# Kernel tuning notes

Measured on AMD Instinct MI355X. Metric: run time of the kernel, lower is better.

## Reference

```python
import jax, jax.numpy as jnp
import numpy as np

S = 160                 # image size (renderer default is 256; reduced for working-set budget)
SIGMA = 1.0             # soft-silhouette sharpness, in pixels
EPS = 1e-8
CHUNK = 512             # faces per rasterization chunk
ANGLE = np.pi / 2.0
VIEW_TAN = float(np.tan(np.radians(30.0)))   # nr.Renderer default viewing_angle=30
CAM_POS = np.array([0.0, 0.0, 2.732], dtype=np.float32)

# constant rotation: Rodrigues formula for axis-angle (pi/2 about y), as in nr.rotation_from_axis
_aa = ANGLE * np.array([0.0, 1.0, 0.0])
_th = np.linalg.norm(_aa)
_k = _aa / _th
_K = np.array([[0, -_k[2], _k[1]], [_k[2], 0, -_k[0]], [-_k[1], _k[0], 0]])
ROT = (np.eye(3) + np.sin(_th) * _K + (1 - np.cos(_th)) * (_K @ _K)).astype(np.float32)


def _make_uv_sphere(stacks=32, slices=64):
    verts = [[0.0, 0.0, 1.0]]
    for i in range(1, stacks):
        phi = np.pi * i / stacks
        for j in range(slices):
            th = 2 * np.pi * j / slices
            verts.append([np.sin(phi) * np.cos(th), np.sin(phi) * np.sin(th), np.cos(phi)])
    verts.append([0.0, 0.0, -1.0])
    V = len(verts)
    faces = []
    for j in range(slices):
        faces.append([0, 1 + j, 1 + (j + 1) % slices])
    for i in range(stacks - 2):
        r0 = 1 + i * slices
        r1 = r0 + slices
        for j in range(slices):
            a, b = r0 + j, r0 + (j + 1) % slices
            c, d = r1 + j, r1 + (j + 1) % slices
            faces.append([a, b, c])
            faces.append([b, d, c])
    r0 = 1 + (stacks - 2) * slices
    for j in range(slices):
        faces.append([V - 1, r0 + (j + 1) % slices, r0 + j])
    return np.asarray(verts, np.float32), np.asarray(faces, np.int32)


def setup_inputs() -> dict:
    key = jax.random.key(0)
    v, f = _make_uv_sphere()                     # V=1986, F=3968
    pad = 4096 - f.shape[0]
    f = np.concatenate([f, np.zeros((pad, 3), np.int32)], axis=0)  # degenerate pad faces
    image_ref = jax.random.uniform(key, (1, S, S), dtype=jnp.float32)
    return {"vertices": jnp.asarray(v)[None], "faces": jnp.asarray(f)[None], "image_ref": image_ref}


def _project(v):
    # world -> camera (rotate, place camera at z=2.732) -> perspective -> pixel coords
    vc = v @ ROT.T + CAM_POS                     # [V,3]
    xy = vc[:, :2] / (vc[:, 2:3] * VIEW_TAN)     # NDC in [-1,1]
    return (xy + 1.0) * (S / 2.0)                # [V,2] pixels


def _soft_coverage(pts, fv):
    # pts [P,2] pixel centers, fv [C,3,2] screen-space triangles -> coverage [P,C]
    a, b, c = fv[:, 0], fv[:, 1], fv[:, 2]

    def edge_dist(p0, p1):
        d = p1 - p0                                              # [C,2]
        cr = d[:, 0] * (pts[:, None, 1] - p0[None, :, 1]) - d[:, 1] * (pts[:, None, 0] - p0[None, :, 0])
        return cr / (jnp.sqrt(jnp.sum(d * d, -1)) + EPS)         # signed pixel distance [P,C]

    area = (b[:, 0] - a[:, 0]) * (c[:, 1] - a[:, 1]) - (b[:, 1] - a[:, 1]) * (c[:, 0] - a[:, 0])
    sg = jnp.where(area >= 0, 1.0, -1.0)[None, :]                # winding correction
    dmin = jnp.minimum(jnp.minimum(edge_dist(a, b) * sg, edge_dist(b, c) * sg), edge_dist(c, a) * sg)
    cov = jax.nn.sigmoid(dmin / SIGMA)
    return cov * (jnp.abs(area) > 1e-6)[None, :]                 # mask degenerate (padded) faces


def reference(vertices, faces, image_ref):
    v2 = _project(vertices[0])                   # [V,2]
    fv = v2[faces[0]]                            # [F,3,2]
    fvc = fv.reshape(-1, CHUNK, 3, 2)            # [F/CHUNK, CHUNK, 3, 2]
    ys, xs = jnp.meshgrid(jnp.arange(S, dtype=jnp.float32) + 0.5,
                          jnp.arange(S, dtype=jnp.float32) + 0.5, indexing="ij")
    pts = jnp.stack([xs.ravel(), ys.ravel()], -1)  # [P,2]

    cov_fn = jax.checkpoint(_soft_coverage)

    def body(not_cov, fvk):
        cov = cov_fn(pts, fvk)                   # [P,CHUNK]
        return not_cov * jnp.prod(1.0 - cov, axis=1), None

    not_cov, _ = jax.lax.scan(body, jnp.ones((S * S,), jnp.float32), fvc)
    images = (1.0 - not_cov).reshape(1, S, S)    # silhouette in [0,1]
    loss = jnp.sum((images - image_ref) ** 2)    # broadcast matches images - image_ref[None] in torch
    return images, loss
```

## Files before the change

kernel.cpp:

```cpp
#include <hip/hip_runtime.h>
#include <math.h>

#define S_IMG 160
#define NPIX (S_IMG * S_IMG)
#define NF 4096
#define NV 1986
#define TS 16
#define NTX 10
#define NTILE 100
#define CAP NF
#define INV_LN2 1.4426950408889634f
#define CULL_THRESH -25.0f

#define ROT_EPS 6.123234e-17f
#define CAM_Z 2.732f
#define VIEW_TAN 0.5773502691896258f

#if __has_builtin(__builtin_amdgcn_exp2f)
#define EXP2F(x) __builtin_amdgcn_exp2f(x)
#else
#define EXP2F(x) exp2f(x)
#endif

__global__ void __launch_bounds__(512) mega(const float* __restrict__ verts,
                                            const int* __restrict__ faces,
                                            float* __restrict__ list,
                                            const float* __restrict__ img_ref,
                                            float* __restrict__ out,
                                            float* __restrict__ bsums) {
    __shared__ float2 sverts[NV];
    __shared__ float4 stage[8][64 * 3];
    __shared__ float pacc[8][256];
    __shared__ float red[8];
    __shared__ int wcnt[8];

    const int t = blockIdx.x;
    const int tid = threadIdx.x;
    const int wid = tid >> 6;
    const int lane = tid & 63;

    for (int i = tid; i < NV; i += 512) {
        float x = verts[3 * i], y = verts[3 * i + 1], z = verts[3 * i + 2];
        float vx = fmaf(ROT_EPS, x, z);
        float vz = fmaf(ROT_EPS, z, -x) + CAM_Z;
        float inv = __builtin_amdgcn_rcpf(vz * VIEW_TAN);
        sverts[i] = make_float2(fmaf(vx * inv, 80.0f, 80.0f),
                                fmaf(y * inv, 80.0f, 80.0f));
    }
    __syncthreads();

    const float cx = (float)((t % NTX) * TS) + 8.0f;
    const float cy = (float)((t / NTX) * TS) + 8.0f;
    float* mylist = list + (size_t)t * CAP * 12;
    int base = 0;

    for (int r = 0; r < NF / 512; ++r) {
        int f = r * 512 + tid;
        int i0 = faces[3 * f], i1 = faces[3 * f + 1], i2 = faces[3 * f + 2];
        float2 a = sverts[i0];
        float2 b = sverts[i1];
        float2 c = sverts[i2];
        float area = (b.x - a.x) * (c.y - a.y) - (b.y - a.y) * (c.x - a.x);
        float sg = (area >= 0.0f) ? INV_LN2 : -INV_LN2;
        bool valid = fabsf(area) > 1e-6f;

        float o[9];
        float umin = 1e30f;
        float2 p0s[3] = {a, b, c};
        float2 p1s[3] = {b, c, a};
#pragma unroll
        for (int e = 0; e < 3; ++e) {
            float dx = p1s[e].x - p0s[e].x;
            float dy = p1s[e].y - p0s[e].y;
            float dd = fmaf(dx, dx, dy * dy);
            float s = sg * __builtin_amdgcn_rsqf(dd);
            float A = valid ? (-dy * s) : 0.0f;
            float B = valid ? (dx * s) : 0.0f;
            float C = valid ? ((dy * p0s[e].x - dx * p0s[e].y) * s) : -1e30f;
            o[3 * e + 0] = A;
            o[3 * e + 1] = B;
            o[3 * e + 2] = C;
            float bound = fmaf(fabsf(A) + fabsf(B), 7.5f, fmaf(A, cx, fmaf(B, cy, C)));
            umin = fminf(umin, valid ? bound : -1e30f);
        }
        bool pred = umin >= CULL_THRESH;
        unsigned long long m = __ballot(pred);
        int wpop = __popcll(m);
        int prefix = __popcll(m & ((1ull << lane) - 1ull));

        __syncthreads();
        if (lane == 0) wcnt[wid] = wpop;
        __syncthreads();
        int off = base;
#pragma unroll
        for (int w = 0; w < 8; ++w) {
            int cw = wcnt[w];
            if (w < wid) off += cw;
            base += cw;
        }
        off += prefix;
        if (pred) {
            float4* dst = (float4*)(mylist + (size_t)off * 12);
            dst[0] = make_float4(o[0], o[1], o[2], o[3]);
            dst[1] = make_float4(o[4], o[5], o[6], o[7]);
            dst[2] = make_float4(o[8], 0.0f, 0.0f, 0.0f);
        }
    }
    __syncthreads();

    const int cnt = base;
    const int nkt = (cnt + 63) >> 6;
    {
        int padcnt = nkt * 64 - cnt;
        for (int i = tid; i < padcnt; i += 512) {
            float4* dst = (float4*)(mylist + (size_t)(cnt + i) * 12);
            dst[0] = make_float4(0.0f, 0.0f, -64.0f, 0.0f);
            dst[1] = make_float4(0.0f, -64.0f, 0.0f, 0.0f);
            dst[2] = make_float4(-64.0f, 0.0f, 0.0f, 0.0f);
        }
    }
    __syncthreads();

    const int colL = lane & 15;
    const int rowL = (lane >> 4) * 4;
    const float px = (float)((t % NTX) * TS + colL) + 0.5f;
    const float py0 = (float)((t / NTX) * TS + rowL) + 0.5f;
    const float py1 = py0 + 1.0f, py2 = py0 + 2.0f, py3 = py0 + 3.0f;

    float P0 = 1.0f, P1 = 1.0f, P2 = 1.0f, P3 = 1.0f;
    float4* myslot = stage[wid];

    for (int k = wid; k < nkt; k += 8) {
        const float4* src = (const float4*)(mylist + (size_t)k * 64 * 12);
#pragma unroll
        for (int i = 0; i < 3; ++i) myslot[lane + i * 64] = src[lane + i * 64];
        asm volatile("s_waitcnt lgkmcnt(0)" ::: "memory");

        for (int j = 0; j < 64; ++j) {
            float4 c0 = myslot[3 * j];
            float4 c1 = myslot[3 * j + 1];
            float4 c2 = myslot[3 * j + 2];
            float b1 = fmaf(c0.x, px, c0.z);
            float b2 = fmaf(c0.w, px, c1.y);
            float b3 = fmaf(c1.z, px, c2.x);
            {
                float d1 = fmaf(c0.y, py0, b1), d2 = fmaf(c1.x, py0, b2), d3 = fmaf(c1.w, py0, b3);
                float e = EXP2F(fminf(fminf(d1, d2), d3));
                P0 = fmaf(P0, e, P0);
            }
            {
                float d1 = fmaf(c0.y, py1, b1), d2 = fmaf(c1.x, py1, b2), d3 = fmaf(c1.w, py1, b3);
                float e = EXP2F(fminf(fminf(d1, d2), d3));
                P1 = fmaf(P1, e, P1);
            }
            {
                float d1 = fmaf(c0.y, py2, b1), d2 = fmaf(c1.x, py2, b2), d3 = fmaf(c1.w, py2, b3);
                float e = EXP2F(fminf(fminf(d1, d2), d3));
                P2 = fmaf(P2, e, P2);
            }
            {
                float d1 = fmaf(c0.y, py3, b1), d2 = fmaf(c1.x, py3, b2), d3 = fmaf(c1.w, py3, b3);
                float e = EXP2F(fminf(fminf(d1, d2), d3));
                P3 = fmaf(P3, e, P3);
            }
        }
        asm volatile("" ::: "memory");
    }

    pacc[wid][rowL * 16 + colL] = __builtin_amdgcn_rcpf(P0);
    pacc[wid][(rowL + 1) * 16 + colL] = __builtin_amdgcn_rcpf(P1);
    pacc[wid][(rowL + 2) * 16 + colL] = __builtin_amdgcn_rcpf(P2);
    pacc[wid][(rowL + 3) * 16 + colL] = __builtin_amdgcn_rcpf(P3);
    __syncthreads();

    float sq = 0.0f;
    if (tid < 256) {
        float prod = 1.0f;
#pragma unroll
        for (int w = 0; w < 8; ++w) prod *= pacc[w][tid];
        float img = 1.0f - prod;
        int col = (t % NTX) * TS + (tid & 15);
        int row = (t / NTX) * TS + (tid >> 4);
        int p = row * S_IMG + col;
        out[p] = img;
        float d = img - img_ref[p];
        sq = d * d;
    }
#pragma unroll
    for (int off = 32; off > 0; off >>= 1) sq += __shfl_down(sq, off);
    if (lane == 0) red[wid] = sq;
    __syncthreads();
    if (tid == 0) {
        float s = ((red[0] + red[1]) + (red[2] + red[3])) +
                  ((red[4] + red[5]) + (red[6] + red[7]));
        bsums[t] = s;
    }
}

__global__ void __launch_bounds__(64) loss_kernel(const float* __restrict__ bsums,
                                                  float* __restrict__ loss_out) {
    int lane = threadIdx.x;
    float v = 0.0f;
    if (lane < NTILE) v = bsums[lane];
    if (lane + 64 < NTILE) v += bsums[lane + 64];
#pragma unroll
    for (int off = 32; off > 0; off >>= 1) v += __shfl_down(v, off);
    if (lane == 0) loss_out[0] = v;
}

extern "C" void kernel_launch(void* const* d_in, const int* in_sizes, int n_in,
                              void* d_out, int out_size, void* d_ws, size_t ws_size,
                              hipStream_t stream) {
    const float* verts = (const float*)d_in[0];
    const int* faces = (const int*)d_in[1];
    const float* img_ref = (const float*)d_in[2];
    float* out = (float*)d_out;

    float* list = (float*)d_ws;
    float* bsums = list + (size_t)NTILE * CAP * 12;

    mega<<<NTILE, 512, 0, stream>>>(verts, faces, list, img_ref, out, bsums);
    loss_kernel<<<1, 64, 0, stream>>>(bsums, out + NPIX);
}
```

Before: 39.17 us.

## Split fused rasterizer into cull, split-K coverage, and finish kernels

```diff
diff --git a/kernel.cpp b/kernel.cpp
--- a/kernel.cpp
+++ b/kernel.cpp
@@ -9,6 +9,7 @@
 #define NTX 10
 #define NTILE 100
 #define CAP NF
+#define SPLIT 16
 #define INV_LN2 1.4426950408889634f
 #define CULL_THRESH -25.0f
 
@@ -22,16 +23,11 @@
 #define EXP2F(x) exp2f(x)
 #endif
 
-__global__ void __launch_bounds__(512) mega(const float* __restrict__ verts,
-                                            const int* __restrict__ faces,
-                                            float* __restrict__ list,
-                                            const float* __restrict__ img_ref,
-                                            float* __restrict__ out,
-                                            float* __restrict__ bsums) {
+__global__ void __launch_bounds__(512) setup_cull(const float* __restrict__ verts,
+                                                  const int* __restrict__ faces,
+                                                  float* __restrict__ list,
+                                                  int* __restrict__ nk_arr) {
     __shared__ float2 sverts[NV];
-    __shared__ float4 stage[8][64 * 3];
-    __shared__ float pacc[8][256];
-    __shared__ float red[8];
     __shared__ int wcnt[8];
 
     const int t = blockIdx.x;
@@ -110,17 +106,25 @@
 
     const int cnt = base;
     const int nkt = (cnt + 63) >> 6;
-    {
-        int padcnt = nkt * 64 - cnt;
-        for (int i = tid; i < padcnt; i += 512) {
-            float4* dst = (float4*)(mylist + (size_t)(cnt + i) * 12);
-            dst[0] = make_float4(0.0f, 0.0f, -64.0f, 0.0f);
-            dst[1] = make_float4(0.0f, -64.0f, 0.0f, 0.0f);
-            dst[2] = make_float4(-64.0f, 0.0f, 0.0f, 0.0f);
-        }
-    }
-    __syncthreads();
-
+    int padcnt = nkt * 64 - cnt;
+    for (int i = tid; i < padcnt; i += 512) {
+        float4* dst = (float4*)(mylist + (size_t)(cnt + i) * 12);
+        dst[0] = make_float4(0.0f, 0.0f, -64.0f, 0.0f);
+        dst[1] = make_float4(0.0f, -64.0f, 0.0f, 0.0f);
+        dst[2] = make_float4(-64.0f, 0.0f, 0.0f, 0.0f);
+    }
+    if (tid == 0) nk_arr[t] = nkt;
+}
+
+__global__ void __launch_bounds__(64) cover(const float* __restrict__ list,
+                                            const int* __restrict__ nk_arr,
+                                            float* __restrict__ pacc) {
+    const int t = blockIdx.x;
+    const int s = blockIdx.y;
+    const int nkt = nk_arr[t];
+    if (s >= nkt) return;
+
+    const int lane = threadIdx.x;
     const int colL = lane & 15;
     const int rowL = (lane >> 4) * 4;
     const float px = (float)((t % NTX) * TS + colL) + 0.5f;
@@ -128,18 +132,14 @@
     const float py1 = py0 + 1.0f, py2 = py0 + 2.0f, py3 = py0 + 3.0f;
 
     float P0 = 1.0f, P1 = 1.0f, P2 = 1.0f, P3 = 1.0f;
-    float4* myslot = stage[wid];
-
-    for (int k = wid; k < nkt; k += 8) {
-        const float4* src = (const float4*)(mylist + (size_t)k * 64 * 12);
-#pragma unroll
-        for (int i = 0; i < 3; ++i) myslot[lane + i * 64] = src[lane + i * 64];
-        asm volatile("s_waitcnt lgkmcnt(0)" ::: "memory");
-
+
+    for (int k = s; k < nkt; k += SPLIT) {
+        const float* fptr = list + ((size_t)t * CAP + (size_t)k * 64) * 12;
+#pragma unroll 4
         for (int j = 0; j < 64; ++j) {
-            float4 c0 = myslot[3 * j];
-            float4 c1 = myslot[3 * j + 1];
-            float4 c2 = myslot[3 * j + 2];
+            float4 c0 = *(const float4*)(fptr + 12 * j);
+            float4 c1 = *(const float4*)(fptr + 12 * j + 4);
+            float4 c2 = *(const float4*)(fptr + 12 * j + 8);
             float b1 = fmaf(c0.x, px, c0.z);
             float b2 = fmaf(c0.w, px, c1.y);
             float b3 = fmaf(c1.z, px, c2.x);
@@ -164,37 +164,40 @@
                 P3 = fmaf(P3, e, P3);
             }
         }
-        asm volatile("" ::: "memory");
-    }
-
-    pacc[wid][rowL * 16 + colL] = __builtin_amdgcn_rcpf(P0);
-    pacc[wid][(rowL + 1) * 16 + colL] = __builtin_amdgcn_rcpf(P1);
-    pacc[wid][(rowL + 2) * 16 + colL] = __builtin_amdgcn_rcpf(P2);
-    pacc[wid][(rowL + 3) * 16 + colL] = __builtin_amdgcn_rcpf(P3);
-    __syncthreads();
-
-    float sq = 0.0f;
-    if (tid < 256) {
-        float prod = 1.0f;
-#pragma unroll
-        for (int w = 0; w < 8; ++w) prod *= pacc[w][tid];
-        float img = 1.0f - prod;
-        int col = (t % NTX) * TS + (tid & 15);
-        int row = (t / NTX) * TS + (tid >> 4);
-        int p = row * S_IMG + col;
-        out[p] = img;
-        float d = img - img_ref[p];
-        sq = d * d;
-    }
+    }
+
+    size_t base = ((size_t)t * SPLIT + s) * 256 + (size_t)rowL * 16 + colL;
+    pacc[base] = __builtin_amdgcn_rcpf(P0);
+    pacc[base + 16] = __builtin_amdgcn_rcpf(P1);
+    pacc[base + 32] = __builtin_amdgcn_rcpf(P2);
+    pacc[base + 48] = __builtin_amdgcn_rcpf(P3);
+}
+
+__global__ void __launch_bounds__(256) finish(const float* __restrict__ pacc,
+                                              const int* __restrict__ nk_arr,
+                                              const float* __restrict__ img_ref,
+                                              float* __restrict__ out,
+                                              float* __restrict__ bsums) {
+    const int t = blockIdx.x;
+    const int tid = threadIdx.x;
+    const int ns = min(nk_arr[t], SPLIT);
+    float prod = 1.0f;
+    for (int sI = 0; sI < ns; ++sI) prod *= pacc[((size_t)t * SPLIT + sI) * 256 + tid];
+    float img = 1.0f - prod;
+    int col = (t % NTX) * TS + (tid & 15);
+    int row = (t / NTX) * TS + (tid >> 4);
+    int p = row * S_IMG + col;
+    out[p] = img;
+    float d = img - img_ref[p];
+    float sq = d * d;
 #pragma unroll
     for (int off = 32; off > 0; off >>= 1) sq += __shfl_down(sq, off);
+    __shared__ float red[4];
+    int lane = tid & 63;
+    int wid = tid >> 6;
     if (lane == 0) red[wid] = sq;
     __syncthreads();
-    if (tid == 0) {
-        float s = ((red[0] + red[1]) + (red[2] + red[3])) +
-                  ((red[4] + red[5]) + (red[6] + red[7]));
-        bsums[t] = s;
-    }
+    if (tid == 0) bsums[t] = (red[0] + red[1]) + (red[2] + red[3]);
 }
 
 __global__ void __launch_bounds__(64) loss_kernel(const float* __restrict__ bsums,
@@ -217,8 +220,12 @@
     float* out = (float*)d_out;
 
     float* list = (float*)d_ws;
-    float* bsums = list + (size_t)NTILE * CAP * 12;
-
-    mega<<<NTILE, 512, 0, stream>>>(verts, faces, list, img_ref, out, bsums);
+    float* pacc = list + (size_t)NTILE * CAP * 12;
+    int* nk_arr = (int*)(pacc + (size_t)NTILE * SPLIT * 256);
+    float* bsums = (float*)(nk_arr + 128);
+
+    setup_cull<<<NTILE, 512, 0, stream>>>(verts, faces, list, nk_arr);
+    cover<<<dim3(NTILE, SPLIT), 64, 0, stream>>>(list, nk_arr, pacc);
+    finish<<<NTILE, 256, 0, stream>>>(pacc, nk_arr, img_ref, out, bsums);
     loss_kernel<<<1, 64, 0, stream>>>(bsums, out + NPIX);
 }
```

Measured after the change: 39.35 us. No clear change (+0.4%).
